# Kernel optimization log

Hardware: AMD Instinct MI355X
Metric: run time of the kernel (lower is better)

Reference implementation:

```python
import jax, jax.numpy as jnp
import numpy as np

D_MODEL = 512
TOP_K = 4


def setup_inputs() -> dict:
    key = jax.random.key(0)
    ks = jax.random.split(key, 7)
    B, L, D = 16, 2048, D_MODEL
    s = 1.0 / np.sqrt(D)
    return {
        "x": jax.random.normal(ks[0], (B, L, D), dtype=jnp.float32),
        "Wq": jax.random.uniform(ks[1], (D, D), jnp.float32, -s, s),
        "bq": jax.random.uniform(ks[2], (D,), jnp.float32, -s, s),
        "Wk": jax.random.uniform(ks[3], (D, D), jnp.float32, -s, s),
        "bk": jax.random.uniform(ks[4], (D,), jnp.float32, -s, s),
        "Wv": jax.random.uniform(ks[5], (D, D), jnp.float32, -s, s),
        "bv": jax.random.uniform(ks[6], (D,), jnp.float32, -s, s),
    }


def reference(x, Wq, bq, Wk, bk, Wv, bv):
    B, L, D = x.shape
    # Linear projections (torch Linear: x @ W.T + b)
    Q = jnp.einsum('bld,ed->ble', x, Wq) + bq
    K = jnp.einsum('bld,ed->ble', x, Wk) + bk
    V = jnp.einsum('bld,ed->ble', x, Wv) + bv
    # FFT autocorrelation along time axis
    q_fft = jnp.fft.rfft(Q, axis=1)
    k_fft = jnp.fft.rfft(K, axis=1)
    corr = jnp.fft.irfft(q_fft * jnp.conj(k_fft), n=L, axis=1)  # [B, L, D]
    mean_corr = corr.mean(axis=-1)                               # [B, L]
    topk_vals, topk_idx = jax.lax.top_k(mean_corr, TOP_K)        # [B, K]
    weights = jax.nn.softmax(topk_vals, axis=-1)                 # [B, K]
    # torch.roll(V[b], shifts=lag, dims=0): out[t] = V[b, (t - lag) % L]
    t = jnp.arange(L)
    gather_idx = (t[None, None, :] - topk_idx[:, :, None]) % L   # [B, K, L]
    rolled = V[jnp.arange(B)[:, None, None], gather_idx]         # [B, K, L, D]
    agg = jnp.einsum('bk,bkld->bld', weights, rolled)
    return agg
```

## Files before the change

kernel.cpp:

```cpp
#include <hip/hip_runtime.h>
#include <math.h>

typedef unsigned short u16;
typedef unsigned int   u32;
typedef __attribute__((ext_vector_type(8))) __bf16 bf16x8;
typedef __attribute__((ext_vector_type(4))) float  f32x4;

#define BB 16
#define LL 2048
#define DD 512
#define NF 1025
#define TOPK 4

static const size_t OFF_XB  = 0;
static const size_t OFF_XTB = OFF_XB  + 8388608;
static const size_t OFF_GTB = OFF_XTB + 8388608;
static const size_t OFF_XC  = OFF_GTB + 8388608;
static const size_t OFF_BBM = OFF_XC  + 8388608;
static const size_t OFF_S   = OFF_BBM + 262144;
static const size_t OFF_W   = OFF_S   + (size_t)BB * NF * 2;
static const size_t OFF_I   = OFF_W   + BB * TOPK;

__device__ __forceinline__ u16 f2bf(float f) {
    u32 u = __float_as_uint(f);
    return (u16)((u + 0x7fffu + ((u >> 16) & 1u)) >> 16);
}
__device__ __forceinline__ float bf2f(u16 h) {
    return __uint_as_float(((u32)h) << 16);
}
__device__ __forceinline__ void gload16(const void* g, void* l) {
    __builtin_amdgcn_global_load_lds((const __attribute__((address_space(1))) void*)g,
                                     (__attribute__((address_space(3))) void*)l, 16, 0, 0);
}
__device__ __forceinline__ float2 cmul(float2 u, float2 v) {
    return make_float2(u.x * v.x - u.y * v.y, u.x * v.y + u.y * v.x);
}
__device__ __forceinline__ float2 cadd(float2 u, float2 v) { return make_float2(u.x + v.x, u.y + v.y); }
__device__ __forceinline__ float2 csub(float2 u, float2 v) { return make_float2(u.x - v.x, u.y - v.y); }

__device__ __forceinline__ int P(int i) { return i + (i >> 3); }

template<int M, int SGN, int NT, int TS>
__device__ __forceinline__ void radix4(const float2* __restrict__ src,
                                       float2* __restrict__ dst,
                                       const float2* __restrict__ twl, int tid) {
#pragma unroll
    for (int r = 0; r < 512 / NT; r++) {
        int w = tid + NT * r;
        int k = w & (M - 1);
        int jm = w - k;
        float2 a = src[P(w)], b = src[P(w + 512)], c = src[P(w + 1024)], d = src[P(w + 1536)];
        float2 t0 = cadd(a, c), t1 = csub(a, c), t2 = cadd(b, d), bd = csub(b, d);
        float2 t3 = (SGN > 0) ? make_float2(bd.y, -bd.x)
                              : make_float2(-bd.y, bd.x);
        int o = 4 * jm + k;
        if (M == 512) {
            dst[P(o)]         = cadd(t0, t2);
            dst[P(o + M)]     = cadd(t1, t3);
            dst[P(o + 2 * M)] = csub(t0, t2);
            dst[P(o + 3 * M)] = csub(t1, t3);
        } else {
            float2 T1 = twl[jm >> TS];
            float2 T2 = cmul(T1, T1);
            float2 T3 = cmul(T1, T2);
            dst[P(o)]         = cadd(t0, t2);
            dst[P(o + M)]     = cmul(cadd(t1, t3), T1);
            dst[P(o + 2 * M)] = cmul(csub(t0, t2), T2);
            dst[P(o + 3 * M)] = cmul(csub(t1, t3), T3);
        }
    }
}

__global__ __launch_bounds__(256) void k_pre(const float* __restrict__ x,
                                             const float* __restrict__ Wq,
                                             const float* __restrict__ Wk,
                                             const float* __restrict__ Wv,
                                             u16* __restrict__ xb,
                                             u16* __restrict__ xtb,
                                             u16* __restrict__ Bm,
                                             float* __restrict__ S) {
    __shared__ char sh[16768];
    int bid = blockIdx.x;
    int tid = threadIdx.x;
    if (bid < 64) {
        int g = bid;
        float (*As)[68] = (float(*)[68])sh;
        float (*Bs)[68] = (float(*)[68])(sh + 4352);
        int tx = tid & 15, ty = tid >> 4;
        int m0 = (g & 7) * 64, n0 = (g >> 3) * 64;
        float acc[4][4] = {};
        for (int k0 = 0; k0 < DD; k0 += 16) {
#pragma unroll
            for (int r = 0; r < 4; r++) {
                As[ty][tx + 16 * r] = Wq[(size_t)(k0 + ty) * DD + m0 + tx + 16 * r];
                Bs[ty][tx + 16 * r] = Wk[(size_t)(k0 + ty) * DD + n0 + tx + 16 * r];
            }
            __syncthreads();
#pragma unroll
            for (int k = 0; k < 16; k++) {
                float4 a4 = *(const float4*)&As[k][ty * 4];
                float4 b4 = *(const float4*)&Bs[k][tx * 4];
                float a[4] = {a4.x, a4.y, a4.z, a4.w};
                float b[4] = {b4.x, b4.y, b4.z, b4.w};
#pragma unroll
                for (int i = 0; i < 4; i++)
#pragma unroll
                    for (int j = 0; j < 4; j++) acc[i][j] += a[i] * b[j];
            }
            __syncthreads();
        }
#pragma unroll
        for (int i = 0; i < 4; i++) {
            uint2 o;
            o.x = (u32)f2bf(acc[i][0]) | ((u32)f2bf(acc[i][1]) << 16);
            o.y = (u32)f2bf(acc[i][2]) | ((u32)f2bf(acc[i][3]) << 16);
            *(uint2*)&Bm[(size_t)(m0 + ty * 4 + i) * DD + n0 + tx * 4] = o;
        }
    } else if (bid < 320) {
        int g = bid - 64;
        int i4 = g * 256 + tid;
        float4 w = ((const float4*)Wv)[i4];
        ushort4 o;
        o.x = f2bf(w.x); o.y = f2bf(w.y); o.z = f2bf(w.z); o.w = f2bf(w.w);
        ((ushort4*)(Bm + DD * DD))[i4] = o;
        if (i4 < 8200)
            ((float4*)S)[i4] = make_float4(0.f, 0.f, 0.f, 0.f);
    } else if (bid < 2368) {
        int tb = bid - 320;
        int bx = tb & 15;
        int by = (tb >> 4) & 7;
        int bz = tb >> 7;
        u32* tile32 = (u32*)sh;
        int tx = tid & 7, ty = tid >> 3;
        int d0 = bx * 32, t0 = by * 256;
        const float* ip = x + ((size_t)bz * LL + t0) * DD + d0 + tx * 4;
        float4 va[4], vb[4];
#pragma unroll
        for (int ii = 0; ii < 4; ii++) {
            int h = ty + 32 * ii;
            va[ii] = *(const float4*)&ip[(size_t)(2 * h) * DD];
            vb[ii] = *(const float4*)&ip[(size_t)(2 * h + 1) * DD];
        }
#pragma unroll
        for (int ii = 0; ii < 4; ii++) {
            int h = ty + 32 * ii;
            u32 a0 = f2bf(va[ii].x), a1 = f2bf(va[ii].y), a2 = f2bf(va[ii].z), a3 = f2bf(va[ii].w);
            u32 b0 = f2bf(vb[ii].x), b1 = f2bf(vb[ii].y), b2 = f2bf(vb[ii].z), b3 = f2bf(vb[ii].w);
            tile32[(4 * tx + 0) * 131 + h] = a0 | (b0 << 16);
            tile32[(4 * tx + 1) * 131 + h] = a1 | (b1 << 16);
            tile32[(4 * tx + 2) * 131 + h] = a2 | (b2 << 16);
            tile32[(4 * tx + 3) * 131 + h] = a3 | (b3 << 16);
        }
        __syncthreads();
        u16* xtp = xtb + ((size_t)bz * DD + d0) * LL + t0;
#pragma unroll
        for (int u = 0; u < 4; u++) {
            int idx = u * 256 + tid;
            int dr = idx >> 5;
            int ch = idx & 31;
            const u32* rp = tile32 + dr * 131 + ch * 4;
            uint4 o = make_uint4(rp[0], rp[1], rp[2], rp[3]);
            *(uint4*)&xtp[(size_t)dr * LL + ch * 8] = o;
        }
    } else {
        size_t g = (size_t)(bid - 2368) * 256 + tid;
        const float4* x4 = (const float4*)x;
        float4 a = x4[2 * g], b = x4[2 * g + 1];
        uint4 o;
        o.x = (u32)f2bf(a.x) | ((u32)f2bf(a.y) << 16);
        o.y = (u32)f2bf(a.z) | ((u32)f2bf(a.w) << 16);
        o.z = (u32)f2bf(b.x) | ((u32)f2bf(b.y) << 16);
        o.w = (u32)f2bf(b.z) | ((u32)f2bf(b.w) << 16);
        ((uint4*)xb)[g] = o;
    }
}

__global__ __launch_bounds__(256, 2) void k_gemm2(const u16* __restrict__ Ab,
                                                  const u16* __restrict__ Bm,
                                                  u16* __restrict__ GTB) {
    __shared__ u16 smem[16384];
    u16* As = smem;
    u16* Bs = smem + 8192;
    int t = threadIdx.x;
    int wave = t >> 6, lane = t & 63;
    int l15 = lane & 15, l4 = lane >> 4;
    int qr = wave & 1, qc = wave >> 1;
    int m0 = blockIdx.x * 128, n0 = blockIdx.y * 128;

    f32x4 acc[4][4];
#pragma unroll
    for (int i = 0; i < 4; i++)
#pragma unroll
        for (int j = 0; j < 4; j++) acc[i][j] = (f32x4){0.f, 0.f, 0.f, 0.f};

    const u16* Ag = Ab + (size_t)m0 * DD;
    const u16* Bg = Bm + (size_t)n0 * DD;
    int a_base = (qr * 64 + l15) * 64 + l4 * 8;
    int b_base = (qc * 64 + l15) * 64 + l4 * 8;

    for (int k0 = 0; k0 < DD; k0 += 64) {
#pragma unroll
        for (int n = 0; n < 4; n++) {
            int c = wave * 256 + n * 64 + lane;
            int row = c >> 3, col = (c & 7) * 8;
            gload16(Ag + (size_t)row * DD + k0 + col, (char*)As + (size_t)(wave * 256 + n * 64) * 16);
            gload16(Bg + (size_t)row * DD + k0 + col, (char*)Bs + (size_t)(wave * 256 + n * 64) * 16);
        }
        __syncthreads();
#pragma unroll
        for (int kk = 0; kk < 64; kk += 32) {
            bf16x8 af[4], bq[4];
#pragma unroll
            for (int i = 0; i < 4; i++) af[i] = *(const bf16x8*)(As + a_base + i * 1024 + kk);
#pragma unroll
            for (int j = 0; j < 4; j++) bq[j] = *(const bf16x8*)(Bs + b_base + j * 1024 + kk);
#pragma unroll
            for (int i = 0; i < 4; i++)
#pragma unroll
                for (int j = 0; j < 4; j++)
                    acc[i][j] = __builtin_amdgcn_mfma_f32_16x16x32_bf16(af[i], bq[j], acc[i][j], 0, 0, 0);
        }
        __syncthreads();
    }

    float4* tb4 = (float4*)smem;
    int bidx = m0 >> 11;
    int tbase = m0 & 2047;
#pragma unroll
    for (int p = 0; p < 2; p++) {
        __syncthreads();
        if (qc == p) {
#pragma unroll
            for (int j = 0; j < 4; j++) {
                int nloc = j * 16 + l15;
#pragma unroll
                for (int i = 0; i < 4; i++) {
                    int tq = qr * 16 + i * 4 + l4;
                    tb4[nloc * 32 + (tq ^ (nloc & 31))] = *(float4*)&acc[i][j];
                }
            }
        }
        __syncthreads();
#pragma unroll
        for (int u = 0; u < 8; u++) {
            int idx4 = u * 256 + t;
            int nloc = idx4 >> 5, c4 = idx4 & 31;
            float4 v = tb4[nloc * 32 + (c4 ^ (nloc & 31))];
            uint2 o;
            o.x = (u32)f2bf(v.x) | ((u32)f2bf(v.y) << 16);
            o.y = (u32)f2bf(v.z) | ((u32)f2bf(v.w) << 16);
            *(uint2*)&GTB[((size_t)bidx * DD + n0 + p * 64 + nloc) * LL + tbase + c4 * 4] = o;
        }
    }
}

__global__ __launch_bounds__(256, 2) void k_gemm3(const u16* __restrict__ Ab,
                                                  const u16* __restrict__ Bm,
                                                  const float* __restrict__ bv,
                                                  float* __restrict__ out) {
    __shared__ u16 smem[16384];
    u16* As = smem;
    u16* Bs = smem + 8192;
    int t = threadIdx.x;
    int wave = t >> 6, lane = t & 63;
    int l15 = lane & 15, l4 = lane >> 4;
    int qr = wave & 1, qc = wave >> 1;
    int m0 = blockIdx.x * 128, n0 = blockIdx.y * 128;

    f32x4 acc[4][4];
#pragma unroll
    for (int i = 0; i < 4; i++)
#pragma unroll
        for (int j = 0; j < 4; j++) acc[i][j] = (f32x4){0.f, 0.f, 0.f, 0.f};

    const u16* Ag = Ab + (size_t)m0 * DD;
    const u16* Bg = Bm + (size_t)DD * DD + (size_t)n0 * DD;
    int a_base = (qr * 64 + l15) * 64 + l4 * 8;
    int b_base = (qc * 64 + l15) * 64 + l4 * 8;

    for (int k0 = 0; k0 < DD; k0 += 64) {
#pragma unroll
        for (int n = 0; n < 4; n++) {
            int c = wave * 256 + n * 64 + lane;
            int row = c >> 3, col = (c & 7) * 8;
            gload16(Ag + (size_t)row * DD + k0 + col, (char*)As + (size_t)(wave * 256 + n * 64) * 16);
            gload16(Bg + (size_t)row * DD + k0 + col, (char*)Bs + (size_t)(wave * 256 + n * 64) * 16);
        }
        __syncthreads();
#pragma unroll
        for (int kk = 0; kk < 64; kk += 32) {
            bf16x8 af[4], bq[4];
#pragma unroll
            for (int i = 0; i < 4; i++) af[i] = *(const bf16x8*)(As + a_base + i * 1024 + kk);
#pragma unroll
            for (int j = 0; j < 4; j++) bq[j] = *(const bf16x8*)(Bs + b_base + j * 1024 + kk);
#pragma unroll
            for (int i = 0; i < 4; i++)
#pragma unroll
                for (int j = 0; j < 4; j++)
                    acc[i][j] = __builtin_amdgcn_mfma_f32_16x16x32_bf16(af[i], bq[j], acc[i][j], 0, 0, 0);
        }
        __syncthreads();
    }

    float*  tb  = (float*)smem;
    float4* tb4 = (float4*)smem;
#pragma unroll
    for (int p = 0; p < 2; p++) {
        __syncthreads();
        if (qr == p) {
#pragma unroll
            for (int j = 0; j < 4; j++) {
                int nloc = qc * 64 + j * 16 + l15;
#pragma unroll
                for (int i = 0; i < 4; i++) {
#pragma unroll
                    for (int r = 0; r < 4; r++) {
                        int mloc = i * 16 + l4 * 4 + r;
                        int nc = ((nloc >> 2) ^ (mloc & 31)) << 2;
                        tb[mloc * 128 + nc + (nloc & 3)] = acc[i][j][r];
                    }
                }
            }
        }
        __syncthreads();
#pragma unroll
        for (int u = 0; u < 8; u++) {
            int idx4 = u * 256 + t;
            int mloc = idx4 >> 5, c4 = idx4 & 31;
            float4 v = tb4[mloc * 32 + (c4 ^ (mloc & 31))];
            float4 bias = *(const float4*)&bv[n0 + c4 * 4];
            v.x += bias.x; v.y += bias.y; v.z += bias.z; v.w += bias.w;
            *(float4*)&out[(size_t)(m0 + p * 64 + mloc) * DD + n0 + c4 * 4] = v;
        }
    }
}

__global__ __launch_bounds__(256) void k_fft(const u16* __restrict__ XTB,
                                             const u16* __restrict__ GTB,
                                             float* __restrict__ S) {
    __shared__ float2 lds[4670];
    float2* b1  = lds;
    float2* b2  = lds + 2303;
    float2* twl = lds + 4606;
    int tid = threadIdx.x;
    int grp = blockIdx.x;
    int b = blockIdx.y;

    if (tid < 64) {
        float sn, cs;
        sincosf(-6.283185307179586f / 2048.0f * (float)(8 * tid), &sn, &cs);
        twl[tid] = make_float2(cs, sn);
    }
    float2 tw;
    {
        float sn, cs;
        sincosf(-6.283185307179586f / 2048.0f * (float)tid, &sn, &cs);
        tw = make_float2(cs, sn);
    }
    const float2 Cm1 = make_float2(0.70710678118654752f, -0.70710678118654752f);
    const float2 Cm2 = make_float2(0.f, -1.f);
    const float2 Cm3 = make_float2(-0.70710678118654752f, -0.70710678118654752f);
    float2 Tm1 = cmul(tw, Cm1), Tm2 = cmul(tw, Cm2), Tm3 = cmul(tw, Cm3);
    float2 R1 = cmul(tw, tw);
    float2 R2 = cmul(R1, R1);
    float2 R3 = cmul(R1, R2);
    __syncthreads();

    float2 sr[4];
#pragma unroll
    for (int r = 0; r < 4; r++) sr[r] = make_float2(0.f, 0.f);
    float s1024 = 0.f;

    for (int c = 0; c < 8; c++) {
        int d = grp * 8 + c;
        const u16* xp = XTB + ((size_t)b * DD + d) * LL;
        const u16* gp = GTB + ((size_t)b * DD + d) * LL;
        float2 se0[4], se1[4];
#pragma unroll
        for (int m = 0; m < 4; m++) {
            int j = tid + 256 * m;
            float2 za = make_float2(bf2f(xp[j]), bf2f(gp[j]));
            float2 zb = make_float2(bf2f(xp[j + 1024]), bf2f(gp[j + 1024]));
            se0[m] = cadd(za, zb);
            float2 dz = csub(za, zb);
            se1[m] = (m == 0) ? cmul(dz, tw)
                   : (m == 1) ? cmul(dz, Tm1)
                   : (m == 2) ? cmul(dz, Tm2)
                              : cmul(dz, Tm3);
        }
        float2* wp = &b1[P(8 * tid)];
        {
            float2 t0 = cadd(se0[0], se0[2]), t1 = csub(se0[0], se0[2]);
            float2 t2 = cadd(se0[1], se0[3]), bd = csub(se0[1], se0[3]);
            float2 t3 = make_float2(bd.y, -bd.x);
            wp[0] = cadd(t0, t2);
            wp[2] = cmul(cadd(t1, t3), R1);
            wp[4] = cmul(csub(t0, t2), R2);
            wp[6] = cmul(csub(t1, t3), R3);
        }
        {
            float2 t0 = cadd(se1[0], se1[2]), t1 = csub(se1[0], se1[2]);
            float2 t2 = cadd(se1[1], se1[3]), bd = csub(se1[1], se1[3]);
            float2 t3 = make_float2(bd.y, -bd.x);
            wp[1] = cadd(t0, t2);
            wp[3] = cmul(cadd(t1, t3), R1);
            wp[5] = cmul(csub(t0, t2), R2);
            wp[7] = cmul(csub(t1, t3), R3);
        }
        __syncthreads();
        radix4<8,   1, 256, 3>(b1, b2, twl, tid); __syncthreads();
        radix4<32,  1, 256, 3>(b2, b1, twl, tid); __syncthreads();
        radix4<128, 1, 256, 3>(b1, b2, twl, tid); __syncthreads();
        radix4<512, 1, 256, 3>(b2, b1, twl, tid); __syncthreads();
#pragma unroll
        for (int r = 0; r < 4; r++) {
            int f = tid + 256 * r;
            float2 p = b1[P(f)];
            float2 q = b1[P((2048 - f) & 2047)];
            float ar = 0.5f * (p.x + q.x), ai = 0.5f * (p.y - q.y);
            float dr = p.x - q.x, di = p.y + q.y;
            float gr = 0.5f * di, gi = -0.5f * dr;
            sr[r].x += ar * gr + ai * gi;
            sr[r].y += ai * gr - ar * gi;
        }
        if (tid == 0) {
            float2 p = b1[P(1024)];
            s1024 += p.x * p.y;
        }
        __syncthreads();
    }
    float* Sg = S + (size_t)b * NF * 2;
#pragma unroll
    for (int r = 0; r < 4; r++) {
        int f = tid + 256 * r;
        atomicAdd(&Sg[2 * f], sr[r].x);
        atomicAdd(&Sg[2 * f + 1], sr[r].y);
    }
    if (tid == 0) {
        atomicAdd(&Sg[2048], s1024);
    }
}

__global__ __launch_bounds__(256) void k_topk(const float* __restrict__ S,
                                              float* __restrict__ wts,
                                              int* __restrict__ idxs) {
    __shared__ float2 lds[5118];
    float2* b1  = lds;
    float2* b2  = lds + 2303;
    float2* twl = lds + 4606;
    __shared__ float cv[2048];
    __shared__ float rv[256];
    __shared__ int ri[256];
    __shared__ float topv[TOPK];
    __shared__ int topi[TOPK];
    int tid = threadIdx.x;
    int b = blockIdx.x;
    const float* Sg = S + (size_t)b * NF * 2;

    for (int j = tid; j < 512; j += 256) {
        float sn, cs;
        sincosf(6.283185307179586f / 2048.0f * (float)j, &sn, &cs);
        twl[j] = make_float2(cs, sn);
    }
    __syncthreads();

#pragma unroll
    for (int h = 0; h < 2; h++) {
#pragma unroll
        for (int e = 0; e < 2; e++) {
            int j = 2 * tid + 512 * h + e;
            float sn, cs;
            sincosf(6.283185307179586f / 2048.0f * (float)j, &sn, &cs);
            float2 T = make_float2(cs, sn);
            float2 zl = make_float2(Sg[2 * j], Sg[2 * j + 1]);
            int fh = j + 1024;
            int ms = 2048 - fh;
            float2 zh = (fh == 1024) ? make_float2(Sg[2048], Sg[2049])
                                     : make_float2(Sg[2 * ms], -Sg[2 * ms + 1]);
            b1[P(2 * j)]     = cadd(zl, zh);
            b1[P(2 * j + 1)] = cmul(csub(zl, zh), T);
        }
    }
    __syncthreads();
    radix4<2,   -1, 256, 0>(b1, b2, twl, tid); __syncthreads();
    radix4<8,   -1, 256, 0>(b2, b1, twl, tid); __syncthreads();
    radix4<32,  -1, 256, 0>(b1, b2, twl, tid); __syncthreads();
    radix4<128, -1, 256, 0>(b2, b1, twl, tid); __syncthreads();
    radix4<512, -1, 256, 0>(b1, b2, twl, tid); __syncthreads();
    const float scale = 1.0f / ((float)LL * (float)DD);
    for (int f = tid; f < 2048; f += 256) cv[f] = b2[P(f)].x * scale;
    __syncthreads();
    for (int r = 0; r < TOPK; r++) {
        float best = -3.0e38f;
        int bi = 0x7fffffff;
        for (int f = tid; f < 2048; f += 256) {
            bool taken = false;
            for (int q = 0; q < r; q++) taken |= (topi[q] == f);
            float v = cv[f];
            if (!taken && (v > best || (v == best && f < bi))) { best = v; bi = f; }
        }
        rv[tid] = best; ri[tid] = bi;
        __syncthreads();
        for (int s = 128; s > 0; s >>= 1) {
            if (tid < s) {
                float v2 = rv[tid + s]; int i2 = ri[tid + s];
                if (v2 > rv[tid] || (v2 == rv[tid] && i2 < ri[tid])) { rv[tid] = v2; ri[tid] = i2; }
            }
            __syncthreads();
        }
        if (tid == 0) { topv[r] = rv[0]; topi[r] = ri[0]; }
        __syncthreads();
    }
    if (tid == 0) {
        float mx = topv[0];
        float e[TOPK], sum = 0.f;
        for (int k = 0; k < TOPK; k++) { e[k] = expf(topv[k] - mx); sum += e[k]; }
        for (int k = 0; k < TOPK; k++) {
            wts[b * TOPK + k] = e[k] / sum;
            idxs[b * TOPK + k] = topi[k];
        }
    }
}

__global__ __launch_bounds__(128) void k_combine(const u16* __restrict__ XB,
                                                 const float* __restrict__ wts,
                                                 const int* __restrict__ idxs,
                                                 u16* __restrict__ XC) {
    int l = blockIdx.x, b = blockIdx.y;
    int t = threadIdx.x;
    const ushort4* Xb = (const ushort4*)(XB + (size_t)b * LL * DD);
    float4 acc = make_float4(0.f, 0.f, 0.f, 0.f);
#pragma unroll
    for (int k = 0; k < TOPK; k++) {
        float w = wts[b * TOPK + k];
        int r = (l - idxs[b * TOPK + k]) & (LL - 1);
        ushort4 v = Xb[(size_t)r * 128 + t];
        acc.x += w * bf2f(v.x); acc.y += w * bf2f(v.y);
        acc.z += w * bf2f(v.z); acc.w += w * bf2f(v.w);
    }
    ushort4 o;
    o.x = f2bf(acc.x); o.y = f2bf(acc.y); o.z = f2bf(acc.z); o.w = f2bf(acc.w);
    ((ushort4*)(XC + (size_t)b * LL * DD))[(size_t)l * 128 + t] = o;
}

extern "C" void kernel_launch(void* const* d_in, const int* in_sizes, int n_in,
                              void* d_out, int out_size, void* d_ws, size_t ws_size,
                              hipStream_t stream) {
    const float* x  = (const float*)d_in[0];
    const float* Wq = (const float*)d_in[1];
    const float* Wk = (const float*)d_in[3];
    const float* Wv = (const float*)d_in[5];
    const float* bv = (const float*)d_in[6];
    (void)in_sizes; (void)n_in; (void)out_size; (void)ws_size;

    float* ws  = (float*)d_ws;
    u16*   XB  = (u16*)(ws + OFF_XB);
    u16*   XTB = (u16*)(ws + OFF_XTB);
    u16*   GTB = (u16*)(ws + OFF_GTB);
    u16*   XC  = (u16*)(ws + OFF_XC);
    u16*   BM  = (u16*)(ws + OFF_BBM);
    float* S   = ws + OFF_S;
    float* wts = ws + OFF_W;
    int*   idx = (int*)(ws + OFF_I);
    float* out = (float*)d_out;

    k_pre<<<10560, 256, 0, stream>>>(x, Wq, Wk, Wv, XB, XTB, BM, S);
    k_gemm2<<<dim3((BB * LL) / 128, DD / 128), 256, 0, stream>>>(XB, BM, GTB);
    k_fft<<<dim3(64, BB), 256, 0, stream>>>(XTB, GTB, S);
    k_topk<<<BB, 256, 0, stream>>>(S, wts, idx);
    k_combine<<<dim3(LL, BB), 128, 0, stream>>>(XB, wts, idx, XC);
    k_gemm3<<<dim3((BB * LL) / 128, DD / 128), 256, 0, stream>>>(XC, BM, bv, out);
}
```

Before: 304.8 us.

## Fuse weighted lag-combine into final GEMM A-tile loading

Removes the separate k_combine kernel and its XC intermediate buffer. The final GEMM now builds its A tile in registers by gathering four lag-shifted rows of XB, weighting them, and writing the bf16 result to shared memory. This avoids one launch and a full write plus re-read of a 16 MB intermediate. In exchange, each of the four N-blocks recomputes the combine, so there are four times the XB reads and more ALU work, and the A load switches from async direct-to-LDS loads to synchronous register loads.

```diff
diff --git a/kernel.cpp b/kernel.cpp
--- a/kernel.cpp
+++ b/kernel.cpp
@@ -256,6 +256,8 @@
 
 __global__ __launch_bounds__(256, 2) void k_gemm3(const u16* __restrict__ Ab,
                                                   const u16* __restrict__ Bm,
+                                                  const float* __restrict__ wts,
+                                                  const int* __restrict__ idxs,
                                                   const float* __restrict__ bv,
                                                   float* __restrict__ out) {
     __shared__ u16 smem[16384];
@@ -266,6 +268,13 @@
     int l15 = lane & 15, l4 = lane >> 4;
     int qr = wave & 1, qc = wave >> 1;
     int m0 = blockIdx.x * 128, n0 = blockIdx.y * 128;
+    int bb = m0 >> 11;
+    int t0 = m0 & 2047;
+
+    float w0 = wts[bb * TOPK + 0], w1 = wts[bb * TOPK + 1];
+    float w2 = wts[bb * TOPK + 2], w3 = wts[bb * TOPK + 3];
+    int dx0 = idxs[bb * TOPK + 0], dx1 = idxs[bb * TOPK + 1];
+    int dx2 = idxs[bb * TOPK + 2], dx3 = idxs[bb * TOPK + 3];
 
     f32x4 acc[4][4];
 #pragma unroll
@@ -273,7 +282,7 @@
 #pragma unroll
         for (int j = 0; j < 4; j++) acc[i][j] = (f32x4){0.f, 0.f, 0.f, 0.f};
 
-    const u16* Ag = Ab + (size_t)m0 * DD;
+    const u16* XBb = Ab + (size_t)bb * LL * DD;
     const u16* Bg = Bm + (size_t)DD * DD + (size_t)n0 * DD;
     int a_base = (qr * 64 + l15) * 64 + l4 * 8;
     int b_base = (qc * 64 + l15) * 64 + l4 * 8;
@@ -283,22 +292,45 @@
         for (int n = 0; n < 4; n++) {
             int c = wave * 256 + n * 64 + lane;
             int row = c >> 3, col = (c & 7) * 8;
-            gload16(Ag + (size_t)row * DD + k0 + col, (char*)As + (size_t)(wave * 256 + n * 64) * 16);
             gload16(Bg + (size_t)row * DD + k0 + col, (char*)Bs + (size_t)(wave * 256 + n * 64) * 16);
         }
+#pragma unroll
+        for (int n = 0; n < 4; n++) {
+            int c = wave * 256 + n * 64 + lane;
+            int row = c >> 3, col = (c & 7) * 8;
+            int tr = t0 + row;
+            float af[8] = {0.f, 0.f, 0.f, 0.f, 0.f, 0.f, 0.f, 0.f};
+#pragma unroll
+            for (int j = 0; j < TOPK; j++) {
+                int dxj = (j == 0) ? dx0 : (j == 1) ? dx1 : (j == 2) ? dx2 : dx3;
+                float wj = (j == 0) ? w0 : (j == 1) ? w1 : (j == 2) ? w2 : w3;
+                int sr = (tr - dxj) & (LL - 1);
+                uint4 v = *(const uint4*)&XBb[(size_t)sr * DD + k0 + col];
+                af[0] += wj * bf2f((u16)v.x);      af[1] += wj * bf2f((u16)(v.x >> 16));
+                af[2] += wj * bf2f((u16)v.y);      af[3] += wj * bf2f((u16)(v.y >> 16));
+                af[4] += wj * bf2f((u16)v.z);      af[5] += wj * bf2f((u16)(v.z >> 16));
+                af[6] += wj * bf2f((u16)v.w);      af[7] += wj * bf2f((u16)(v.w >> 16));
+            }
+            uint4 o;
+            o.x = (u32)f2bf(af[0]) | ((u32)f2bf(af[1]) << 16);
+            o.y = (u32)f2bf(af[2]) | ((u32)f2bf(af[3]) << 16);
+            o.z = (u32)f2bf(af[4]) | ((u32)f2bf(af[5]) << 16);
+            o.w = (u32)f2bf(af[6]) | ((u32)f2bf(af[7]) << 16);
+            *(uint4*)((char*)As + (size_t)c * 16) = o;
+        }
         __syncthreads();
 #pragma unroll
         for (int kk = 0; kk < 64; kk += 32) {
-            bf16x8 af[4], bq[4];
-#pragma unroll
-            for (int i = 0; i < 4; i++) af[i] = *(const bf16x8*)(As + a_base + i * 1024 + kk);
+            bf16x8 af4[4], bq[4];
+#pragma unroll
+            for (int i = 0; i < 4; i++) af4[i] = *(const bf16x8*)(As + a_base + i * 1024 + kk);
 #pragma unroll
             for (int j = 0; j < 4; j++) bq[j] = *(const bf16x8*)(Bs + b_base + j * 1024 + kk);
 #pragma unroll
             for (int i = 0; i < 4; i++)
 #pragma unroll
                 for (int j = 0; j < 4; j++)
-                    acc[i][j] = __builtin_amdgcn_mfma_f32_16x16x32_bf16(af[i], bq[j], acc[i][j], 0, 0, 0);
+                    acc[i][j] = __builtin_amdgcn_mfma_f32_16x16x32_bf16(af4[i], bq[j], acc[i][j], 0, 0, 0);
         }
         __syncthreads();
     }
@@ -523,27 +555,6 @@
     }
 }
 
-__global__ __launch_bounds__(128) void k_combine(const u16* __restrict__ XB,
-                                                 const float* __restrict__ wts,
-                                                 const int* __restrict__ idxs,
-                                                 u16* __restrict__ XC) {
-    int l = blockIdx.x, b = blockIdx.y;
-    int t = threadIdx.x;
-    const ushort4* Xb = (const ushort4*)(XB + (size_t)b * LL * DD);
-    float4 acc = make_float4(0.f, 0.f, 0.f, 0.f);
-#pragma unroll
-    for (int k = 0; k < TOPK; k++) {
-        float w = wts[b * TOPK + k];
-        int r = (l - idxs[b * TOPK + k]) & (LL - 1);
-        ushort4 v = Xb[(size_t)r * 128 + t];
-        acc.x += w * bf2f(v.x); acc.y += w * bf2f(v.y);
-        acc.z += w * bf2f(v.z); acc.w += w * bf2f(v.w);
-    }
-    ushort4 o;
-    o.x = f2bf(acc.x); o.y = f2bf(acc.y); o.z = f2bf(acc.z); o.w = f2bf(acc.w);
-    ((ushort4*)(XC + (size_t)b * LL * DD))[(size_t)l * 128 + t] = o;
-}
-
 extern "C" void kernel_launch(void* const* d_in, const int* in_sizes, int n_in,
                               void* d_out, int out_size, void* d_ws, size_t ws_size,
                               hipStream_t stream) {
@@ -558,7 +569,6 @@
     u16*   XB  = (u16*)(ws + OFF_XB);
     u16*   XTB = (u16*)(ws + OFF_XTB);
     u16*   GTB = (u16*)(ws + OFF_GTB);
-    u16*   XC  = (u16*)(ws + OFF_XC);
     u16*   BM  = (u16*)(ws + OFF_BBM);
     float* S   = ws + OFF_S;
     float* wts = ws + OFF_W;
@@ -569,6 +579,5 @@
     k_gemm2<<<dim3((BB * LL) / 128, DD / 128), 256, 0, stream>>>(XB, BM, GTB);
     k_fft<<<dim3(64, BB), 256, 0, stream>>>(XTB, GTB, S);
     k_topk<<<BB, 256, 0, stream>>>(S, wts, idx);
-    k_combine<<<dim3(LL, BB), 128, 0, stream>>>(XB, wts, idx, XC);
-    k_gemm3<<<dim3((BB * LL) / 128, DD / 128), 256, 0, stream>>>(XC, BM, bv, out);
-}
+    k_gemm3<<<dim3((BB * LL) / 128, DD / 128), 256, 0, stream>>>(XB, BM, wts, idx, bv, out);
+}
```

New measurement: 363.7 us. 1.19x slower.
